# Optimization experiments

Measured on AMD Instinct MI355X. Metric: run time of the kernel, lower is better.

Reference implementation:

```python
import jax, jax.numpy as jnp
import numpy as np

B, S, D = 2, 1024, 4096
N_HEADS, KV_HEADS, HEAD_DIM = 32, 8, 128
EPS = 1e-6
ROPE_THETA = 1e6


def setup_inputs() -> dict:
    key = jax.random.key(0)
    ks = jax.random.split(key, 7)
    scale = 0.02
    x = jax.random.normal(ks[0], (B, S, D), dtype=jnp.float32)
    positions = jnp.broadcast_to(jnp.arange(S, dtype=jnp.int32)[None, :], (B, S))
    wq = jax.random.normal(ks[1], (D, N_HEADS, HEAD_DIM), dtype=jnp.float32) * scale
    wk = jax.random.normal(ks[2], (D, KV_HEADS, HEAD_DIM), dtype=jnp.float32) * scale
    wv = jax.random.normal(ks[3], (D, KV_HEADS, HEAD_DIM), dtype=jnp.float32) * scale
    wo = jax.random.normal(ks[4], (N_HEADS, HEAD_DIM, D), dtype=jnp.float32) * scale
    q_norm_w = 1.0 + jax.random.normal(ks[5], (HEAD_DIM,), dtype=jnp.float32) * 0.01
    k_norm_w = 1.0 + jax.random.normal(ks[6], (HEAD_DIM,), dtype=jnp.float32) * 0.01
    return {"x": x, "positions": positions, "wq": wq, "wk": wk, "wv": wv,
            "wo": wo, "q_norm_w": q_norm_w, "k_norm_w": k_norm_w}


def _rms_norm(t, w):
    # per-head RMSNorm over last (head_dim) axis
    var = jnp.mean(jnp.square(t), axis=-1, keepdims=True)
    return (t * jax.lax.rsqrt(var + EPS)) * w


def _rope(t, positions):
    # neox-style rotary embedding; t: [B, S, n, H], positions: [B, S]
    half = t.shape[-1] // 2
    inv_freq = 1.0 / (ROPE_THETA ** (jnp.arange(0, half, dtype=jnp.float32) / half))
    ang = positions.astype(jnp.float32)[..., None] * inv_freq  # [B, S, half]
    cos = jnp.cos(ang)[:, :, None, :]  # [B, S, 1, half]
    sin = jnp.sin(ang)[:, :, None, :]
    t1, t2 = t[..., :half], t[..., half:]
    return jnp.concatenate([t1 * cos - t2 * sin, t2 * cos + t1 * sin], axis=-1)


def reference(x, positions, wq, wk, wv, wo, q_norm_w, k_norm_w):
    # QKV projections (einsum layers: 'bsd,dnh->bsnh')
    q = jnp.einsum('bsd,dnh->bsnh', x, wq)  # [B, S, N, H]
    k = jnp.einsum('bsd,dkh->bskh', x, wk)  # [B, S, K, H]
    v = jnp.einsum('bsd,dkh->bskh', x, wv)
    # per-head QK RMSNorm, then RoPE
    q = _rope(_rms_norm(q, q_norm_w), positions)
    k = _rope(_rms_norm(k, k_norm_w), positions)
    # GQA: expand KV heads to query heads
    groups = N_HEADS // KV_HEADS
    k = jnp.repeat(k, groups, axis=2)  # [B, S, N, H]
    v = jnp.repeat(v, groups, axis=2)
    sm_scale = HEAD_DIM ** -0.5
    scores = jnp.einsum('bqnh,btnh->bnqt', q, k) * sm_scale  # [B, N, S, S]
    causal = jnp.tril(jnp.ones((S, S), dtype=bool))
    scores = jnp.where(causal[None, None], scores, jnp.finfo(scores.dtype).min)
    probs = jax.nn.softmax(scores, axis=-1)
    attn = jnp.einsum('bnqt,btnh->bqnh', probs, v)  # [B, S, N, H]
    out = jnp.einsum('bqnh,nhd->bqd', attn, wo)  # output projection
    return out
```

## Files before the change

### kernel.cpp

```cpp
#include <hip/hip_runtime.h>
#include <stdint.h>

#define S_LEN   1024
#define D_MODEL 4096
#define NHQ     32
#define NKV     8
#define HD      128
#define NTOK    2048
#define NQKV    6144
#define SM_SCALE 0.08838834764831843f

typedef __attribute__((ext_vector_type(8))) __bf16 bf16x8;
typedef __attribute__((ext_vector_type(4))) float f32x4;

__device__ __forceinline__ unsigned short f2bf(float f) {
  union { float f; unsigned u; } x; x.f = f;
  unsigned r = x.u + 0x7fffu + ((x.u >> 16) & 1u);
  return (unsigned short)(r >> 16);
}
__device__ __forceinline__ float bf2f(unsigned short u) {
  union { unsigned u; float f; } x; x.u = (unsigned)u << 16; return x.f;
}

__device__ __forceinline__ void gload_lds16(const void* g, void* l) {
  __builtin_amdgcn_global_load_lds((__attribute__((address_space(1))) void*)g,
                                   (__attribute__((address_space(3))) void*)l,
                                   16, 0, 0);
}

__global__ void k_f32_to_bf16(const float* __restrict__ in,
                              unsigned short* __restrict__ out, int n8) {
  int i = blockIdx.x * blockDim.x + threadIdx.x;
  if (i >= n8) return;
  const float4* p = (const float4*)(in + (size_t)i * 8);
  float4 v0 = p[0], v1 = p[1];
  uint4 o;
  o.x = f2bf(v0.x) | ((unsigned)f2bf(v0.y) << 16);
  o.y = f2bf(v0.z) | ((unsigned)f2bf(v0.w) << 16);
  o.z = f2bf(v1.x) | ((unsigned)f2bf(v1.y) << 16);
  o.w = f2bf(v1.z) | ((unsigned)f2bf(v1.w) << 16);
  *(uint4*)(out + (size_t)i * 8) = o;
}

__global__ void k_transpose(const float* __restrict__ in,
                            unsigned short* __restrict__ out, int R, int C) {
  __shared__ float t[32][33];
  int c = threadIdx.x & 31, r0 = threadIdx.x >> 5;
  int cb = blockIdx.x * 32, rb = blockIdx.y * 32;
#pragma unroll
  for (int i = 0; i < 4; ++i) {
    int r = r0 + i * 8;
    t[r][c] = in[(size_t)(rb + r) * C + cb + c];
  }
  __syncthreads();
#pragma unroll
  for (int i = 0; i < 4; ++i) {
    int r = r0 + i * 8;
    out[(size_t)(cb + r) * R + rb + c] = f2bf(t[c][r]);
  }
}


#define STGA(ksrc, half, bufi)                                                  \
  { int kcl = (ksrc) < NT ? (ksrc) : NT - 1;                                    \
    _Pragma("unroll")                                                           \
    for (int i_ = 0; i_ < 2; ++i_) {                                            \
      int lin = i_ * 512 + tid;                                                 \
      int r_ = lin >> 2, slot = lin & 3;                                        \
      int sw = slot ^ ((r_ >> 1) & 3);                                          \
      gload_lds16(Aptr + (size_t)(bm + r_) * Kstride + kcl * 64 + (half) * 32 + sw * 8, \
                  smem + (bufi) * BUFST + (half) * 16384 + lin * 16);           \
    } }

#define STGB(ksrc, half, bufi)                                                  \
  { int kcl = (ksrc) < NT ? (ksrc) : NT - 1;                                    \
    _Pragma("unroll")                                                           \
    for (int i_ = 0; i_ < NF / 2; ++i_) {                                       \
      int lin = i_ * 512 + tid;                                                 \
      int r_ = lin >> 2, slot = lin & 3;                                        \
      int sw = slot ^ ((r_ >> 1) & 3);                                          \
      gload_lds16(Bptr + (size_t)(bn + r_) * Kstride + kcl * 64 + (half) * 32 + sw * 8, \
                  smem + (bufi) * BUFST + 32768 + (half) * (NF * 4096) + lin * 16); \
    } }

#define RD_A(mh, kh, bufi)                                                      \
  _Pragma("unroll")                                                             \
  for (int mf = 0; mf < 4; ++mf) {                                              \
    int row = wr * 128 + (mh) * 64 + mf * 16 + lr;                              \
    af[mf] = *(const bf16x8*)(smem + (bufi) * BUFST + (kh) * 16384 + row * 64   \
                              + ((lg * 16) ^ (((row >> 1) & 3) << 4)));         \
  }

#define RD_B(kh, bufi)                                                          \
  _Pragma("unroll")                                                             \
  for (int nf = 0; nf < NF; ++nf) {                                             \
    int row = wc * NF * 16 + nf * 16 + lr;                                      \
    bf[nf] = *(const bf16x8*)(smem + (bufi) * BUFST + 32768 + (kh) * (NF * 4096) \
                              + row * 64 + ((lg * 16) ^ (((row >> 1) & 3) << 4))); \
  }

#define GATEW                                                                   \
  { if constexpr (NF == 4) asm volatile("s_waitcnt vmcnt(4)" ::: "memory");     \
    else                   asm volatile("s_waitcnt vmcnt(3)" ::: "memory"); }

#define PHASE_TAIL(mh, GATE)                                                    \
  if (GATE) GATEW                                                               \
  __builtin_amdgcn_s_barrier();                                                 \
  asm volatile("s_waitcnt lgkmcnt(0)" ::: "memory");                            \
  __builtin_amdgcn_sched_barrier(0);                                            \
  __builtin_amdgcn_s_setprio(1);                                                \
  _Pragma("unroll")                                                             \
  for (int mf = 0; mf < 4; ++mf)                                                \
    _Pragma("unroll")                                                           \
    for (int nf = 0; nf < NF; ++nf)                                             \
      acc[(mh) * 4 + mf][nf] = __builtin_amdgcn_mfma_f32_16x16x32_bf16(         \
          af[mf], bf[nf], acc[(mh) * 4 + mf][nf], 0, 0, 0);                     \
  __builtin_amdgcn_s_setprio(0);                                                \
  __builtin_amdgcn_s_barrier();

template <int NF, typename OutT>
__global__ __launch_bounds__(512, 1) void k_gemm256(
    const unsigned short* __restrict__ Aptr,
    const unsigned short* __restrict__ Bptr,
    OutT* __restrict__ C, int Kstride, int ldc, int NT, int SGN, int nxn) {
  extern __shared__ __align__(16) char smem[];
  constexpr int BUFST = 32768 + NF * 8192;
  int tid = threadIdx.x;
  int l = tid & 63;
  int w = tid >> 6;
  int lr = l & 15, lg = l >> 4;
  int wr = w >> 2, wc = w & 3;
  int per_xcd = gridDim.x >> 3;
  int x8 = blockIdx.x & 7, i = blockIdx.x >> 3;
  int SGM = per_xcd / SGN;
  int xr = x8 / nxn, xc = x8 - xr * nxn;
  int iy = i / SGN;
  int by = xr * SGM + iy, bx = xc * SGN + (i - iy * SGN);
  int bm = by * 256, bn = bx * NF * 64;

  f32x4 acc[8][NF] = {};
  bf16x8 af[4], bf[NF];

  STGA(0, 0, 0) STGB(0, 0, 0)
  STGA(0, 1, 0) STGB(0, 1, 0)
  GATEW
  __builtin_amdgcn_s_barrier();

  for (int kt = 0; kt < NT; ++kt) {
    int cur = kt & 1;
    RD_A(0, 0, cur) RD_B(0, cur)
    STGA(kt + 1, 0, cur ^ 1)
    PHASE_TAIL(0, 0)
    RD_A(1, 0, cur)
    STGB(kt + 1, 0, cur ^ 1)
    PHASE_TAIL(1, 1)
    RD_A(0, 1, cur) RD_B(1, cur)
    STGA(kt + 1, 1, cur ^ 1)
    PHASE_TAIL(0, 0)
    RD_A(1, 1, cur)
    STGB(kt + 1, 1, cur ^ 1)
    PHASE_TAIL(1, 1)
  }

#pragma unroll
  for (int mh = 0; mh < 2; ++mh)
#pragma unroll
    for (int mf = 0; mf < 4; ++mf)
#pragma unroll
      for (int nf = 0; nf < NF; ++nf)
#pragma unroll
        for (int j = 0; j < 4; ++j) {
          size_t idx = (size_t)(bm + wr * 128 + mh * 64 + mf * 16 + lg * 4 + j) * ldc +
                       bn + wc * NF * 16 + nf * 16 + lr;
          float v = acc[mh * 4 + mf][nf][j];
          if constexpr (sizeof(OutT) == 2) C[idx] = f2bf(v);
          else C[idx] = v;
        }
}

__global__ void k_norm_rope(const unsigned short* __restrict__ qkv,
                            const float* __restrict__ w,
                            const int* __restrict__ positions,
                            unsigned short* __restrict__ out, int nheads, int colbase,
                            float oscale) {
  int wid = blockIdx.x * 4 + (threadIdx.x >> 6);
  int lane = threadIdx.x & 63;
  int token = wid / nheads, head = wid - token * nheads;
  const unsigned short* src = qkv + (size_t)token * NQKV + colbase + head * HD;
  float e0 = bf2f(src[lane]), e1 = bf2f(src[lane + 64]);
  float ss = e0 * e0 + e1 * e1;
#pragma unroll
  for (int m = 1; m < 64; m <<= 1) ss += __shfl_xor(ss, m, 64);
  float rs = rsqrtf(ss * (1.0f / 128.0f) + 1e-6f);
  float n0 = e0 * rs * w[lane], n1 = e1 * rs * w[lane + 64];
  int pos = positions[token];
  float invf = exp2f((float)lane * (-19.931568569324174f / 64.0f));
  float ang = (float)pos * invf;
  float sv, cv;
  sincosf(ang, &sv, &cv);
  float o0 = (n0 * cv - n1 * sv) * oscale;
  float o1 = (n1 * cv + n0 * sv) * oscale;
  int b = token >> 10, s = token & 1023;
  size_t ob = ((size_t)(b * nheads + head) * S_LEN + s) * HD;
  out[ob + lane] = f2bf(o0);
  out[ob + 64 + lane] = f2bf(o1);
}

__global__ void k_v_transpose(const unsigned short* __restrict__ qkv,
                              unsigned short* __restrict__ vt) {
  __shared__ unsigned short t[32][33];
  int slice = blockIdx.z;
  int b = slice >> 3, kh = slice & 7;
  const unsigned short* in = qkv + (size_t)(b * S_LEN) * NQKV + 5120 + kh * HD;
  unsigned short* out = vt + (size_t)slice * HD * S_LEN;
  int c = threadIdx.x & 31, r0 = threadIdx.x >> 5;
  int s0 = blockIdx.y * 32, d0 = blockIdx.x * 32;
#pragma unroll
  for (int i = 0; i < 4; ++i) {
    int r = r0 + i * 8;
    t[r][c] = in[(size_t)(s0 + r) * NQKV + d0 + c];
  }
  __syncthreads();
#pragma unroll
  for (int i = 0; i < 4; ++i) {
    int r = r0 + i * 8;
    out[(size_t)(d0 + r) * S_LEN + s0 + c] = t[c][r];
  }
}

__global__ __launch_bounds__(256) void k_attn(const unsigned short* __restrict__ qh,
                                              const unsigned short* __restrict__ kbuf,
                                              const unsigned short* __restrict__ vtbuf,
                                              unsigned short* __restrict__ attn_out) {
  __shared__ __align__(16) unsigned short k_lds[64 * 128];
  __shared__ __align__(16) unsigned short v_lds[128 * 64];
  __shared__ __align__(16) unsigned short p_lds[4][16 * 64];
  int b = blockIdx.z, h = blockIdx.y, bx = blockIdx.x;
  int khd = h >> 2;
  int tid = threadIdx.x, w = tid >> 6, l = tid & 63;
  int lr = l & 15, lg = l >> 4;
  const unsigned short* K = kbuf + (size_t)(b * NKV + khd) * S_LEN * HD;
  const unsigned short* VT = vtbuf + (size_t)(b * NKV + khd) * HD * S_LEN;
  char* klp = (char*)k_lds;
  char* vlp = (char*)v_lds;
  char* plp = (char*)p_lds[w];
  int swz = (lr & 7) << 4;

  for (int strip = 0; strip < 2; ++strip) {
    int qs = strip ? (15 - bx) : bx;
    int q0 = qs * 64;
    const unsigned short* Q = qh + ((size_t)(b * NHQ + h) * S_LEN + q0 + w * 16) * HD;
    bf16x8 qf[4];
#pragma unroll
    for (int kk = 0; kk < 4; ++kk)
      qf[kk] = *(const bf16x8*)&Q[(size_t)lr * HD + kk * 32 + lg * 8];

    f32x4 o[8] = {};
    float m_[4], l_[4];
#pragma unroll
    for (int j = 0; j < 4; ++j) { m_[j] = -1e30f; l_[j] = 0.0f; }

    int nt = qs + 1;
    for (int t = 0; t < nt; ++t) {
      int t0 = t * 64;
      __syncthreads();
#pragma unroll
      for (int it = 0; it < 4; ++it) {
        int db = (tid + it * 256) * 16;
        int kr = db >> 8, kc = db & 255;
        gload_lds16(K + (size_t)(t0 + kr) * HD + ((kc ^ ((kr & 7) << 4)) >> 1), klp + db);
        int vr = db >> 7, vc = db & 127;
        gload_lds16(VT + (size_t)vr * S_LEN + t0 + ((vc ^ ((vr & 7) << 4)) >> 1), vlp + db);
      }
      __syncthreads();

      f32x4 sc[4];
      __builtin_amdgcn_s_setprio(1);
#pragma unroll
      for (int ct = 0; ct < 4; ++ct) {
        f32x4 s = {};
        int row = ct * 16 + lr;
#pragma unroll
        for (int kk = 0; kk < 4; ++kk) {
          bf16x8 kf = *(const bf16x8*)(klp + row * 256 + ((kk * 64 + lg * 16) ^ swz));
          s = __builtin_amdgcn_mfma_f32_16x16x32_bf16(qf[kk], kf, s, 0, 0, 0);
        }
        sc[ct] = s;
      }
      __builtin_amdgcn_s_setprio(0);

      bool full = (t < qs);
      float alpha[4];
#pragma unroll
      for (int j = 0; j < 4; ++j) {
        if (!full) {
          int rg = q0 + w * 16 + lg * 4 + j;
#pragma unroll
          for (int ct = 0; ct < 4; ++ct)
            sc[ct][j] = (t0 + ct * 16 + lr <= rg) ? sc[ct][j] : -1e30f;
        }
        float mx = fmaxf(fmaxf(sc[0][j], sc[1][j]), fmaxf(sc[2][j], sc[3][j]));
#pragma unroll
        for (int msk = 1; msk < 16; msk <<= 1) mx = fmaxf(mx, __shfl_xor(mx, msk, 64));
        float mn = fmaxf(m_[j], mx);
        alpha[j] = __expf(m_[j] - mn);
        int q = lg * 4 + j;
        int psw = (q & 7) << 4;
        float ps = 0.0f;
#pragma unroll
        for (int ct = 0; ct < 4; ++ct) {
          float p = __expf(sc[ct][j] - mn);
          ps += p;
          *(unsigned short*)(plp + q * 128 + (((ct * 16 + lr) * 2) ^ psw)) = f2bf(p);
        }
#pragma unroll
        for (int msk = 1; msk < 16; msk <<= 1) ps += __shfl_xor(ps, msk, 64);
        l_[j] = l_[j] * alpha[j] + ps;
        m_[j] = mn;
      }
#pragma unroll
      for (int dc = 0; dc < 8; ++dc) {
        o[dc][0] *= alpha[0]; o[dc][1] *= alpha[1];
        o[dc][2] *= alpha[2]; o[dc][3] *= alpha[3];
      }
      asm volatile("s_waitcnt lgkmcnt(0)" ::: "memory");
      __builtin_amdgcn_s_setprio(1);
#pragma unroll
      for (int kt = 0; kt < 2; ++kt) {
        bf16x8 pa = *(const bf16x8*)(plp + lr * 128 + ((kt * 64 + lg * 16) ^ swz));
#pragma unroll
        for (int dc = 0; dc < 8; ++dc) {
          int vrow = dc * 16 + lr;
          bf16x8 vf = *(const bf16x8*)(vlp + vrow * 128 + ((kt * 64 + lg * 16) ^ swz));
          o[dc] = __builtin_amdgcn_mfma_f32_16x16x32_bf16(pa, vf, o[dc], 0, 0, 0);
        }
      }
      __builtin_amdgcn_s_setprio(0);
    }

#pragma unroll
    for (int j = 0; j < 4; ++j) {
      int rg = q0 + w * 16 + lg * 4 + j;
      size_t row = (size_t)(b * S_LEN + rg) * D_MODEL + h * HD;
      float inv = 1.0f / l_[j];
#pragma unroll
      for (int dc = 0; dc < 8; ++dc)
        attn_out[row + dc * 16 + lr] = f2bf(o[dc][j] * inv);
    }
  }
}

extern "C" void kernel_launch(void* const* d_in, const int* in_sizes, int n_in,
                              void* d_out, int out_size, void* d_ws, size_t ws_size,
                              hipStream_t stream) {
  const float* x        = (const float*)d_in[0];
  const int* positions  = (const int*)d_in[1];
  const float* wq       = (const float*)d_in[2];
  const float* wk       = (const float*)d_in[3];
  const float* wv       = (const float*)d_in[4];
  const float* wo       = (const float*)d_in[5];
  const float* qnw      = (const float*)d_in[6];
  const float* knw      = (const float*)d_in[7];
  float* out            = (float*)d_out;

  char* ws = (char*)d_ws;
  unsigned short* xb   = (unsigned short*)(ws);
  unsigned short* wB   = (unsigned short*)(ws + 16777216);
  unsigned short* woT  = (unsigned short*)(ws + 67108864);
  unsigned short* qkvb = (unsigned short*)(ws + 100663296);
  unsigned short* qh   = wB;
  unsigned short* khb  = (unsigned short*)(ws + 33554432);
  unsigned short* vtb  = (unsigned short*)(ws + 37748736);
  unsigned short* attn = xb;

  dim3 tb(256);
  k_f32_to_bf16<<<4096, tb, 0, stream>>>(x, xb, 1048576);
  k_transpose<<<dim3(128, 128), tb, 0, stream>>>(wq, wB, 4096, 4096);
  k_transpose<<<dim3(32, 128), tb, 0, stream>>>(wk, wB + (size_t)4096 * 4096, 4096, 1024);
  k_transpose<<<dim3(32, 128), tb, 0, stream>>>(wv, wB + (size_t)5120 * 4096, 4096, 1024);
  k_transpose<<<dim3(128, 128), tb, 0, stream>>>(wo, woT, 4096, 4096);

  k_gemm256<4, unsigned short><<<dim3(192), dim3(512), 131072, stream>>>(
      xb, wB, qkvb, 4096, 6144, 64, 6, 4);

  k_norm_rope<<<16384, tb, 0, stream>>>(qkvb, qnw, positions, qh, 32, 0, SM_SCALE);
  k_norm_rope<<<4096, tb, 0, stream>>>(qkvb, knw, positions, khb, 8, 4096, 1.0f);
  k_v_transpose<<<dim3(4, 32, 16), tb, 0, stream>>>(qkvb, vtb);

  k_attn<<<dim3(8, 32, 2), tb, 0, stream>>>(qh, khb, vtb, attn);

  k_gemm256<2, float><<<dim3(256), dim3(512), 98304, stream>>>(
      attn, woT, out, 4096, 4096, 64, 8, 4);
}
```

Measured before the change: 324.2 us.

## Double-buffer LDS fragment reads ahead of MFMA and retile output GEMM

Restructures the GEMM main loop so the LDS fragment reads for the next phase are issued before the current phase's MFMAs. This uses two register sets for the A and B fragments. Global-to-LDS address computation is hoisted into per-thread precomputed pointers. The tile height is now a template parameter, and the output projection switches from a 256x128 tile to a 128x256 tile with a different grid swizzle. This costs extra registers and barrier choreography in exchange for more overlap between LDS reads and MFMA work.

```diff
diff --git a/kernel.cpp b/kernel.cpp
--- a/kernel.cpp
+++ b/kernel.cpp
@@ -61,70 +61,61 @@
 }
 
 
-#define STGA(ksrc, half, bufi)                                                  \
-  { int kcl = (ksrc) < NT ? (ksrc) : NT - 1;                                    \
-    _Pragma("unroll")                                                           \
-    for (int i_ = 0; i_ < 2; ++i_) {                                            \
-      int lin = i_ * 512 + tid;                                                 \
-      int r_ = lin >> 2, slot = lin & 3;                                        \
-      int sw = slot ^ ((r_ >> 1) & 3);                                          \
-      gload_lds16(Aptr + (size_t)(bm + r_) * Kstride + kcl * 64 + (half) * 32 + sw * 8, \
-                  smem + (bufi) * BUFST + (half) * 16384 + lin * 16);           \
-    } }
-
-#define STGB(ksrc, half, bufi)                                                  \
-  { int kcl = (ksrc) < NT ? (ksrc) : NT - 1;                                    \
-    _Pragma("unroll")                                                           \
-    for (int i_ = 0; i_ < NF / 2; ++i_) {                                       \
-      int lin = i_ * 512 + tid;                                                 \
-      int r_ = lin >> 2, slot = lin & 3;                                        \
-      int sw = slot ^ ((r_ >> 1) & 3);                                          \
-      gload_lds16(Bptr + (size_t)(bn + r_) * Kstride + kcl * 64 + (half) * 32 + sw * 8, \
-                  smem + (bufi) * BUFST + 32768 + (half) * (NF * 4096) + lin * 16); \
-    } }
-
-#define RD_A(mh, kh, bufi)                                                      \
+#define LGKM0 { asm volatile("s_waitcnt lgkmcnt(0)" ::: "memory"); \
+                __builtin_amdgcn_sched_barrier(0); }
+#define SCHED __builtin_amdgcn_sched_barrier(0);
+#define BAR   __builtin_amdgcn_s_barrier();
+#define GATE  { if constexpr (MH + NF / 2 == 4)                                 \
+                  asm volatile("s_waitcnt vmcnt(4)" ::: "memory");              \
+                else                                                            \
+                  asm volatile("s_waitcnt vmcnt(3)" ::: "memory"); }
+
+#define STGA(h, bufb, kOff)                                                     \
+  _Pragma("unroll")                                                             \
+  for (int i_ = 0; i_ < MH; ++i_)                                               \
+    gload_lds16(gA[i_] + (kOff) + (h) * 64,                                     \
+                smem + (bufb) + (h) * (MH * 8192) + dA[i_]);
+
+#define STGB(h, bufb, kOff)                                                     \
+  _Pragma("unroll")                                                             \
+  for (int i_ = 0; i_ < NF / 2; ++i_)                                           \
+    gload_lds16(gB[i_] + (kOff) + (h) * 64,                                     \
+                smem + (bufb) + ABYTES + (h) * (NF * 4096) + dB[i_]);
+
+#define RD_A(dst, mh, kh, bufb)                                                 \
   _Pragma("unroll")                                                             \
   for (int mf = 0; mf < 4; ++mf) {                                              \
-    int row = wr * 128 + (mh) * 64 + mf * 16 + lr;                              \
-    af[mf] = *(const bf16x8*)(smem + (bufi) * BUFST + (kh) * 16384 + row * 64   \
-                              + ((lg * 16) ^ (((row >> 1) & 3) << 4)));         \
-  }
-
-#define RD_B(kh, bufi)                                                          \
+    int row = wr * (MH * 64) + (mh) * 64 + mf * 16 + lr;                        \
+    dst[mf] = *(const bf16x8*)(smem + (bufb) + (kh) * (MH * 8192) + row * 64    \
+                               + ((lg * 16) ^ (((row >> 1) & 3) << 4)));        \
+  }
+
+#define RD_B(dst, kh, bufb)                                                     \
   _Pragma("unroll")                                                             \
   for (int nf = 0; nf < NF; ++nf) {                                             \
-    int row = wc * NF * 16 + nf * 16 + lr;                                      \
-    bf[nf] = *(const bf16x8*)(smem + (bufi) * BUFST + 32768 + (kh) * (NF * 4096) \
-                              + row * 64 + ((lg * 16) ^ (((row >> 1) & 3) << 4))); \
-  }
-
-#define GATEW                                                                   \
-  { if constexpr (NF == 4) asm volatile("s_waitcnt vmcnt(4)" ::: "memory");     \
-    else                   asm volatile("s_waitcnt vmcnt(3)" ::: "memory"); }
-
-#define PHASE_TAIL(mh, GATE)                                                    \
-  if (GATE) GATEW                                                               \
-  __builtin_amdgcn_s_barrier();                                                 \
-  asm volatile("s_waitcnt lgkmcnt(0)" ::: "memory");                            \
-  __builtin_amdgcn_sched_barrier(0);                                            \
+    int row = wc * (NF * 16) + nf * 16 + lr;                                    \
+    dst[nf] = *(const bf16x8*)(smem + (bufb) + ABYTES + (kh) * (NF * 4096)      \
+                               + row * 64 + ((lg * 16) ^ (((row >> 1) & 3) << 4))); \
+  }
+
+#define MFMA16(mh, AF, BF)                                                      \
   __builtin_amdgcn_s_setprio(1);                                                \
   _Pragma("unroll")                                                             \
   for (int mf = 0; mf < 4; ++mf)                                                \
     _Pragma("unroll")                                                           \
     for (int nf = 0; nf < NF; ++nf)                                             \
       acc[(mh) * 4 + mf][nf] = __builtin_amdgcn_mfma_f32_16x16x32_bf16(         \
-          af[mf], bf[nf], acc[(mh) * 4 + mf][nf], 0, 0, 0);                     \
-  __builtin_amdgcn_s_setprio(0);                                                \
-  __builtin_amdgcn_s_barrier();
-
-template <int NF, typename OutT>
+          AF[mf], BF[nf], acc[(mh) * 4 + mf][nf], 0, 0, 0);                     \
+  __builtin_amdgcn_s_setprio(0);
+
+template <int MH, int NF, typename OutT>
 __global__ __launch_bounds__(512, 1) void k_gemm256(
     const unsigned short* __restrict__ Aptr,
     const unsigned short* __restrict__ Bptr,
     OutT* __restrict__ C, int Kstride, int ldc, int NT, int SGN, int nxn) {
   extern __shared__ __align__(16) char smem[];
-  constexpr int BUFST = 32768 + NF * 8192;
+  constexpr int ABYTES = MH * 16384;
+  constexpr int BUFST = MH * 16384 + NF * 8192;
   int tid = threadIdx.x;
   int l = tid & 63;
   int w = tid >> 6;
@@ -136,42 +127,83 @@
   int xr = x8 / nxn, xc = x8 - xr * nxn;
   int iy = i / SGN;
   int by = xr * SGM + iy, bx = xc * SGN + (i - iy * SGN);
-  int bm = by * 256, bn = bx * NF * 64;
-
-  f32x4 acc[8][NF] = {};
-  bf16x8 af[4], bf[NF];
+  int bm = by * (MH * 128), bn = bx * (NF * 64);
+
+  const char* gA[MH]; int dA[MH];
+#pragma unroll
+  for (int i_ = 0; i_ < MH; ++i_) {
+    int lin = i_ * 512 + tid;
+    int r_ = lin >> 2, slot = lin & 3, sw = slot ^ ((r_ >> 1) & 3);
+    gA[i_] = (const char*)(Aptr + (size_t)(bm + r_) * Kstride) + sw * 16;
+    dA[i_] = lin * 16;
+  }
+  const char* gB[NF / 2]; int dB[NF / 2];
+#pragma unroll
+  for (int i_ = 0; i_ < NF / 2; ++i_) {
+    int lin = i_ * 512 + tid;
+    int r_ = lin >> 2, slot = lin & 3, sw = slot ^ ((r_ >> 1) & 3);
+    gB[i_] = (const char*)(Bptr + (size_t)(bn + r_) * Kstride) + sw * 16;
+    dB[i_] = lin * 16;
+  }
+
+  f32x4 acc[MH * 4][NF] = {};
+  bf16x8 afA[4], afB[4], bfA[NF], bfB[NF];
 
   STGA(0, 0, 0) STGB(0, 0, 0)
-  STGA(0, 1, 0) STGB(0, 1, 0)
-  GATEW
-  __builtin_amdgcn_s_barrier();
+  STGA(1, 0, 0) STGB(1, 0, 0)
+  GATE
+  BAR
+  RD_A(afA, 0, 0, 0) RD_B(bfA, 0, 0)
 
   for (int kt = 0; kt < NT; ++kt) {
-    int cur = kt & 1;
-    RD_A(0, 0, cur) RD_B(0, cur)
-    STGA(kt + 1, 0, cur ^ 1)
-    PHASE_TAIL(0, 0)
-    RD_A(1, 0, cur)
-    STGB(kt + 1, 0, cur ^ 1)
-    PHASE_TAIL(1, 1)
-    RD_A(0, 1, cur) RD_B(1, cur)
-    STGA(kt + 1, 1, cur ^ 1)
-    PHASE_TAIL(0, 0)
-    RD_A(1, 1, cur)
-    STGB(kt + 1, 1, cur ^ 1)
-    PHASE_TAIL(1, 1)
-  }
-
-#pragma unroll
-  for (int mh = 0; mh < 2; ++mh)
+    int curb = (kt & 1) * BUFST;
+    int nxtb = BUFST - curb;
+    int kOff = (kt + 1) * 128;
+    if constexpr (MH == 2) {
+      STGA(0, nxtb, kOff)
+      BAR LGKM0
+      RD_A(afB, 1, 0, curb) SCHED
+      MFMA16(0, afA, bfA)
+      BAR
+      STGB(0, nxtb, kOff)
+      GATE BAR LGKM0
+      RD_A(afA, 0, 1, curb) RD_B(bfB, 1, curb) SCHED
+      MFMA16(1, afB, bfA)
+      BAR
+      STGA(1, nxtb, kOff)
+      BAR LGKM0
+      RD_A(afB, 1, 1, curb) SCHED
+      MFMA16(0, afA, bfB)
+      BAR
+      STGB(1, nxtb, kOff)
+      GATE BAR LGKM0
+      RD_A(afA, 0, 0, nxtb) RD_B(bfA, 0, nxtb) SCHED
+      MFMA16(1, afB, bfB)
+      BAR
+    } else {
+      STGA(0, nxtb, kOff) STGB(0, nxtb, kOff)
+      GATE BAR LGKM0
+      RD_A(afB, 0, 1, curb) RD_B(bfB, 1, curb) SCHED
+      MFMA16(0, afA, bfA)
+      BAR
+      STGA(1, nxtb, kOff) STGB(1, nxtb, kOff)
+      GATE BAR LGKM0
+      RD_A(afA, 0, 0, nxtb) RD_B(bfA, 0, nxtb) SCHED
+      MFMA16(0, afB, bfB)
+      BAR
+    }
+  }
+
+#pragma unroll
+  for (int mh = 0; mh < MH; ++mh)
 #pragma unroll
     for (int mf = 0; mf < 4; ++mf)
 #pragma unroll
       for (int nf = 0; nf < NF; ++nf)
 #pragma unroll
         for (int j = 0; j < 4; ++j) {
-          size_t idx = (size_t)(bm + wr * 128 + mh * 64 + mf * 16 + lg * 4 + j) * ldc +
-                       bn + wc * NF * 16 + nf * 16 + lr;
+          size_t idx = (size_t)(bm + wr * (MH * 64) + mh * 64 + mf * 16 + lg * 4 + j) * ldc +
+                       bn + wc * (NF * 16) + nf * 16 + lr;
           float v = acc[mh * 4 + mf][nf][j];
           if constexpr (sizeof(OutT) == 2) C[idx] = f2bf(v);
           else C[idx] = v;
@@ -380,7 +412,7 @@
   k_transpose<<<dim3(32, 128), tb, 0, stream>>>(wv, wB + (size_t)5120 * 4096, 4096, 1024);
   k_transpose<<<dim3(128, 128), tb, 0, stream>>>(wo, woT, 4096, 4096);
 
-  k_gemm256<4, unsigned short><<<dim3(192), dim3(512), 131072, stream>>>(
+  k_gemm256<2, 4, unsigned short><<<dim3(192), dim3(512), 131072, stream>>>(
       xb, wB, qkvb, 4096, 6144, 64, 6, 4);
 
   k_norm_rope<<<16384, tb, 0, stream>>>(qkvb, qnw, positions, qh, 32, 0, SM_SCALE);
@@ -389,6 +421,6 @@
 
   k_attn<<<dim3(8, 32, 2), tb, 0, stream>>>(qh, khb, vtb, attn);
 
-  k_gemm256<2, float><<<dim3(256), dim3(512), 98304, stream>>>(
-      attn, woT, out, 4096, 4096, 64, 8, 4);
-}
+  k_gemm256<1, 4, float><<<dim3(256), dim3(512), 98304, stream>>>(
+      attn, woT, out, 4096, 4096, 64, 4, 4);
+}
```

Measured after the change: 329.8 us. About the same (+1.7%).
